# Kernel tuning notes

Hardware: AMD Instinct MI355X
Metric: run time of the kernel (lower is better)

The kernel has to match this reference:

```python
import jax, jax.numpy as jnp
import numpy as np

B, L, D = 4, 2048, 512
H, DK = 8, 64          # n_heads, d_k = d_model // n_heads
DF = 2048              # d_ff
W = 9                  # window_size (odd so padding w//2 keeps L windows)


def setup_inputs() -> dict:
    key = jax.random.key(0)
    ks = jax.random.split(key, 12)
    s = 0.02
    p = lambda k, shp: (jax.random.normal(k, shp, jnp.float32) * s)
    return {
        "x": jax.random.normal(ks[0], (B, L, D), jnp.float32),
        "Wq": p(ks[1], (D, D)), "bq": jnp.zeros((D,), jnp.float32),
        "Wk": p(ks[2], (D, D)), "bk": jnp.zeros((D,), jnp.float32),
        "Wv": p(ks[3], (D, D)), "bv": jnp.zeros((D,), jnp.float32),
        "Wo": p(ks[4], (D, D)), "bo": jnp.zeros((D,), jnp.float32),
        "W1": p(ks[5], (D, DF)), "b1": jnp.zeros((DF,), jnp.float32),
        "W2": p(ks[6], (DF, D)), "b2": jnp.zeros((D,), jnp.float32),
        "g1": jnp.ones((D,), jnp.float32), "be1": jnp.zeros((D,), jnp.float32),
        "g2": jnp.ones((D,), jnp.float32), "be2": jnp.zeros((D,), jnp.float32),
    }


def _layer_norm(x, g, b, eps=1e-5):
    m = jnp.mean(x, axis=-1, keepdims=True)
    v = jnp.var(x, axis=-1, keepdims=True)
    return (x - m) * jax.lax.rsqrt(v + eps) * g + b


def reference(x, Wq, bq, Wk, bk, Wv, bv, Wo, bo, W1, b1, W2, b2, g1, be1, g2, be2):
    b, l, d = x.shape
    pad = W // 2
    padded = jnp.pad(x, ((0, 0), (pad, pad), (0, 0)))          # (B, L+W-1, D)
    idx = jnp.arange(l)[:, None] + jnp.arange(W)[None, :]       # (L, W)
    win = padded[:, idx]                                        # (B, L, W, D)

    # per-window full attention (Informer FullAttention, mask_flag=False)
    q = (win @ Wq + bq).reshape(b, l, W, H, DK)
    k = (win @ Wk + bk).reshape(b, l, W, H, DK)
    v = (win @ Wv + bv).reshape(b, l, W, H, DK)
    scale = 1.0 / jnp.sqrt(jnp.float32(DK))
    scores = jnp.einsum('blqhe,blkhe->blhqk', q, k) * scale     # (B, L, H, W, W)
    attn = jax.nn.softmax(scores, axis=-1)
    o = jnp.einsum('blhqk,blkhd->blqhd', attn, v).reshape(b, l, W, d)
    o = o @ Wo + bo                                             # (B, L, W, D)
    new_x = jnp.mean(o, axis=2)                                 # mean-pool over window

    x1 = _layer_norm(x + new_x, g1, be1)

    # pointwise conv FFN (kernel_size=1 Conv1d == Linear), exact GELU
    h = jax.nn.gelu(x1 @ W1 + b1, approximate=False)
    y = h @ W2 + b2
    return _layer_norm(x1 + y, g2, be2)
```

## Files before the change

kernel.cpp:

```cpp
#include <hip/hip_runtime.h>


typedef unsigned short u16;
typedef __attribute__((ext_vector_type(8))) short short8;
typedef __attribute__((ext_vector_type(4))) float floatx4;

#define DEV static __device__ __forceinline__

DEV float b2f(u16 u) {
  union { unsigned int i; float f; } x; x.i = ((unsigned int)u) << 16; return x.f;
}
DEV u16 f2b(float f) {
  union { float f; unsigned int i; } x; x.f = f;
  unsigned int u = x.i + 0x7fffu + ((x.i >> 16) & 1u);
  return (u16)(u >> 16);
}

#define AS1 __attribute__((address_space(1)))
#define AS3 __attribute__((address_space(3)))
DEV void gload_lds16(const void* g, void* l) {
  __builtin_amdgcn_global_load_lds((const AS1 void*)g, (AS3 void*)l, 16, 0, 0);
}

__global__ __launch_bounds__(256) void prep_weights(
    const float* __restrict__ Wq, const float* __restrict__ Wk,
    const float* __restrict__ Wo, const float* __restrict__ W1,
    const float* __restrict__ W2, const float* __restrict__ Wv,
    u16* __restrict__ WqkvT, u16* __restrict__ WoT,
    u16* __restrict__ W1T, u16* __restrict__ W2T, u16* __restrict__ Wvb) {
  const int bid = blockIdx.x;
  if (bid >= 2816) {
    const int i = (bid - 2816) * 256 + threadIdx.x;
    float4 v = ((const float4*)Wv)[i];
    ushort4 o;
    o.x = f2b(v.x); o.y = f2b(v.y); o.z = f2b(v.z); o.w = f2b(v.w);
    ((ushort4*)Wvb)[i] = o;
    return;
  }
  const float* in; u16* out; int R, C, t;
  if (bid < 256)       { in = Wq; out = WqkvT;          R = 512;  C = 512;  t = bid; }
  else if (bid < 512)  { in = Wk; out = WqkvT + 262144; R = 512;  C = 512;  t = bid - 256; }
  else if (bid < 768)  { in = Wo; out = WoT;            R = 512;  C = 512;  t = bid - 512; }
  else if (bid < 1792) { in = W1; out = W1T;            R = 512;  C = 2048; t = bid - 768; }
  else                 { in = W2; out = W2T;            R = 2048; C = 512;  t = bid - 1792; }
  const int tpr = C >> 5;
  const int bc = (t % tpr) * 32, br = (t / tpr) * 32;
  __shared__ float tile[32][33];
  const int tx = threadIdx.x & 31, ty = threadIdx.x >> 5;
  #pragma unroll
  for (int i = 0; i < 32; i += 8)
    tile[ty + i][tx] = in[(size_t)(br + ty + i) * C + bc + tx];
  __syncthreads();
  #pragma unroll
  for (int i = 0; i < 32; i += 8)
    out[(size_t)(bc + ty + i) * R + br + tx] = f2b(tile[tx][ty + i]);
}

__global__ __launch_bounds__(256) void bias_prep(
    const float* __restrict__ bq, const float* __restrict__ bk,
    const float* __restrict__ bv, const float* __restrict__ Wo,
    float* __restrict__ o) {
  const int i = blockIdx.x * 256 + threadIdx.x;
  if (i < 512) o[i] = bq[i];
  else if (i < 1024) o[i] = bk[i - 512];
  else if (i < 1536) {
    const int c = i - 1024;
    float s = 0.f;
    for (int j = 0; j < 512; ++j) s += bv[j] * Wo[(size_t)j * 512 + c];
    o[i] = s;
  } else if (i < 2048) o[i] = 0.f;
}

__global__ __launch_bounds__(256) void f2b_vec(
    const float* __restrict__ in, u16* __restrict__ out, int n4) {
  int i = blockIdx.x * 256 + threadIdx.x;
  if (i < n4) {
    float4 v = ((const float4*)in)[i];
    ushort4 o;
    o.x = f2b(v.x); o.y = f2b(v.y); o.z = f2b(v.z); o.w = f2b(v.w);
    ((ushort4*)out)[i] = o;
  }
}

template<int EPI>
__global__ __launch_bounds__(256, 4) void gemm_bt(
    const u16* __restrict__ A, const u16* __restrict__ BT,
    const float* __restrict__ bias, u16* __restrict__ C, u16* __restrict__ C2,
    int M, int N, int lda, int kb) {
  __shared__ __align__(16) u16 As[3][4096];
  __shared__ __align__(16) u16 Bs[3][2048];
  const int tid = threadIdx.x;
  const int w = tid >> 6, l = tid & 63;
  const int l15 = l & 15, l4 = l >> 4;
  const int wr = w & 1, wc = w >> 1;

  const int gx = (int)gridDim.x, gy = (int)gridDim.y;
  int id = ((int)blockIdx.z * gy + (int)blockIdx.y) * gx + (int)blockIdx.x;
  const int nwg = gx * gy * (int)gridDim.z;
  if ((nwg & 7) == 0) { const int cpx = nwg >> 3; id = (id & 7) * cpx + (id >> 3); }
  const int bx = id % gx; const int r1 = id / gx;
  const int by = r1 % gy; const int bz = r1 / gy;
  const int bm = by * 128, bn = bx * 64;
  const int koff = bz * kb;

  const int row0 = tid >> 2;
  const int kc0 = ((((tid & 3) - ((tid >> 3) & 3)) & 3)) * 8;
  const u16* gA = A  + (size_t)(bm + row0) * lda + koff + kc0;
  const u16* gB = BT + (size_t)(bn + row0) * lda + koff + kc0;
  const size_t a1 = (size_t)64 * lda;
  const int sd = w * 512 + l * 8;

  const int rg8 = ((l4 + ((l15 >> 1) & 3)) & 3) * 8;
  const int aBase = (wr * 64 + l15) * 32 + rg8;
  const int bBase = (wc * 32 + l15) * 32 + rg8;

  floatx4 acc[4][2] = {};
  const int nt = kb >> 5;

  auto stage = [&](int t, int buf) {
    const u16* a = gA + (size_t)t * 32;
    const u16* b = gB + (size_t)t * 32;
    gload_lds16(a,      &As[buf][sd]);
    gload_lds16(a + a1, &As[buf][2048 + sd]);
    gload_lds16(b,      &Bs[buf][sd]);
  };

  stage(0, 0);
  stage(1, 1);
  asm volatile("s_waitcnt vmcnt(3)" ::: "memory");
  __builtin_amdgcn_s_barrier();
  asm volatile("" ::: "memory");

  int cur = 0;
  for (int t = 0; t < nt; ++t) {
    int sb = cur + 2; if (sb >= 3) sb -= 3;
    const bool pf = (t + 2 < nt);
    if (pf) stage(t + 2, sb);

    short8 af[4], bf[2];
    #pragma unroll
    for (int m = 0; m < 4; ++m) af[m] = *(const short8*)(&As[cur][aBase + m * 512]);
    #pragma unroll
    for (int n = 0; n < 2; ++n) bf[n] = *(const short8*)(&Bs[cur][bBase + n * 512]);
    #pragma unroll
    for (int m = 0; m < 4; ++m)
      #pragma unroll
      for (int n = 0; n < 2; ++n)
        acc[m][n] = __builtin_amdgcn_mfma_f32_16x16x32_bf16(af[m], bf[n], acc[m][n], 0, 0, 0);

    if (pf) asm volatile("s_waitcnt vmcnt(3)" ::: "memory");
    else    asm volatile("s_waitcnt vmcnt(0)" ::: "memory");
    __builtin_amdgcn_s_barrier();
    asm volatile("" ::: "memory");

    cur = (cur == 2) ? 0 : cur + 1;
  }

  const int col0 = bn + wc * 32 + l15;
  if (EPI <= 1) {
    float bvv[2];
    #pragma unroll
    for (int n = 0; n < 2; ++n) bvv[n] = bias[col0 + n * 16];
    #pragma unroll
    for (int m = 0; m < 4; ++m) {
      #pragma unroll
      for (int ri = 0; ri < 4; ++ri) {
        const size_t row = (size_t)(bm + wr * 64 + m * 16 + l4 * 4 + ri);
        u16* cp = C + row * N + col0;
        #pragma unroll
        for (int n = 0; n < 2; ++n) {
          float vv = acc[m][n][ri] + bvv[n];
          if (EPI == 1) vv = 0.5f * vv * (1.0f + erff(vv * 0.70710678118654752f));
          cp[n * 16] = f2b(vv);
        }
      }
    }
  } else {
    u16* o = (bz == 0) ? C : C2;
    #pragma unroll
    for (int m = 0; m < 4; ++m) {
      #pragma unroll
      for (int ri = 0; ri < 4; ++ri) {
        const size_t row = (size_t)(bm + wr * 64 + m * 16 + l4 * 4 + ri);
        u16* cp = o + row * N + col0;
        #pragma unroll
        for (int n = 0; n < 2; ++n) cp[n * 16] = f2b(acc[m][n][ri]);
      }
    }
  }
}

#define ATL 32
#define ART (ATL + 8)

__global__ __launch_bounds__(256) void attn_band(
    const u16* __restrict__ QKV, const float* __restrict__ bqkv,
    const float* __restrict__ bo, u16* __restrict__ newx) {
  __shared__ __align__(16) u16 S3[3][ART][72];
  __shared__ float Gb[ART][18];
  __shared__ float Sm[ART][81];
  __shared__ float Wb[ATL][9];

  const int tid = threadIdx.x;
  const int bid = ((int)blockIdx.x & 7) * 256 + ((int)blockIdx.x >> 3);
  const int h = bid & 7;
  const int chunk = (bid >> 3) & 63;
  const int b = bid >> 9;
  const int l0 = chunk * ATL;

  for (int idx = tid; idx < ART * 24; idx += 256) {
    const int ti = idx / 24, c = idx % 24;
    const int slice = c >> 3, d8 = (c & 7) * 8;
    const int col = slice * 512 + h * 64 + d8;
    const int t = l0 - 4 + ti;
    short8 v;
    if ((unsigned)t < 2048u) {
      v = *(const short8*)(QKV + ((size_t)((b << 11) | t)) * 1536 + col);
    } else {
      #pragma unroll
      for (int j = 0; j < 8; ++j) v[j] = (short)f2b(bqkv[col + j]);
    }
    *(short8*)(&S3[slice][ti][d8]) = v;
  }
  __syncthreads();

  for (int task = tid; task < ART * 17; task += 256) {
    const int ti = task / 17, j = task % 17;
    const int ui = ti + j - 8;
    if ((unsigned)ui < (unsigned)ART) {
      float a = 0.f;
      #pragma unroll
      for (int d0 = 0; d0 < 64; d0 += 8) {
        short8 qv = *(const short8*)(&S3[0][ti][d0]);
        short8 kv = *(const short8*)(&S3[1][ui][d0]);
        #pragma unroll
        for (int jj = 0; jj < 8; ++jj) a += b2f((u16)qv[jj]) * b2f((u16)kv[jj]);
      }
      Gb[ti][j] = a * 0.125f;
    }
  }
  __syncthreads();

  for (int task = tid; task < ART * 9; task += 256) {
    const int ti = task / 9, qw = task % 9;
    const int li = ti - qw;
    if ((unsigned)li < (unsigned)ATL) {
      float m = -1e30f;
      #pragma unroll
      for (int kw = 0; kw < 9; ++kw) m = fmaxf(m, Gb[ti][kw - qw + 8]);
      float e[9], s = 0.f;
      #pragma unroll
      for (int kw = 0; kw < 9; ++kw) { e[kw] = expf(Gb[ti][kw - qw + 8] - m); s += e[kw]; }
      const float inv = 1.f / s;
      #pragma unroll
      for (int kw = 0; kw < 9; ++kw) Sm[ti][qw * 9 + kw] = e[kw] * inv;
    }
  }
  __syncthreads();

  for (int task = tid; task < ATL * 9; task += 256) {
    const int li = task / 9, kw = task % 9;
    float s = 0.f;
    #pragma unroll
    for (int qw = 0; qw < 9; ++qw) s += Sm[li + qw][qw * 9 + kw];
    Wb[li][kw] = s * (1.f / 9.f);
  }
  __syncthreads();

  {
    const int li = tid >> 3, d8 = (tid & 7) * 8;
    float w[9];
    #pragma unroll
    for (int kw = 0; kw < 9; ++kw) w[kw] = Wb[li][kw];
    float a[8] = {};
    #pragma unroll
    for (int kw = 0; kw < 9; ++kw) {
      short8 vv = *(const short8*)(&S3[2][li + kw][d8]);
      #pragma unroll
      for (int jj = 0; jj < 8; ++jj) a[jj] += w[kw] * b2f((u16)vv[jj]);
    }
    short8 o;
    #pragma unroll
    for (int jj = 0; jj < 8; ++jj) o[jj] = (short)f2b(a[jj] + bo[h * 64 + d8 + jj]);
    const int l = l0 + li;
    *(short8*)(newx + ((size_t)((b << 11) | l)) * 512 + h * 64 + d8) = o;
  }
}

template<int MODE>
__global__ __launch_bounds__(256) void ln_kernel(
    const u16* __restrict__ a, const u16* __restrict__ bsrc,
    const u16* __restrict__ csrc, const float* __restrict__ bias,
    const float* __restrict__ g, const float* __restrict__ be,
    u16* __restrict__ outb, float* __restrict__ outf) {
  const int wave = threadIdx.x >> 6, lane = threadIdx.x & 63;
  const size_t row = (size_t)blockIdx.x * 4 + wave;
  const size_t base = row * 512 + lane * 8;
  const int gi = lane * 8;
  float v[8];
  short8 a8 = *(const short8*)(a + base);
  short8 b8 = *(const short8*)(bsrc + base);
  #pragma unroll
  for (int j = 0; j < 8; ++j) v[j] = b2f((u16)a8[j]) + b2f((u16)b8[j]);
  if (MODE == 1) {
    short8 c8 = *(const short8*)(csrc + base);
    #pragma unroll
    for (int j = 0; j < 8; ++j) v[j] += b2f((u16)c8[j]) + bias[gi + j];
  }

  float s = 0.f;
  #pragma unroll
  for (int j = 0; j < 8; ++j) s += v[j];
  #pragma unroll
  for (int off = 32; off >= 1; off >>= 1) s += __shfl_xor(s, off, 64);
  const float mean = s * (1.f / 512.f);
  float sq = 0.f;
  #pragma unroll
  for (int j = 0; j < 8; ++j) { float d = v[j] - mean; sq += d * d; }
  #pragma unroll
  for (int off = 32; off >= 1; off >>= 1) sq += __shfl_xor(sq, off, 64);
  const float rs = rsqrtf(sq * (1.f / 512.f) + 1e-5f);

  if (MODE == 0) {
    short8 o;
    #pragma unroll
    for (int j = 0; j < 8; ++j)
      o[j] = (short)f2b((v[j] - mean) * rs * g[gi + j] + be[gi + j]);
    *(short8*)(outb + base) = o;
  } else {
    float4 o0, o1;
    o0.x = (v[0] - mean) * rs * g[gi + 0] + be[gi + 0];
    o0.y = (v[1] - mean) * rs * g[gi + 1] + be[gi + 1];
    o0.z = (v[2] - mean) * rs * g[gi + 2] + be[gi + 2];
    o0.w = (v[3] - mean) * rs * g[gi + 3] + be[gi + 3];
    o1.x = (v[4] - mean) * rs * g[gi + 4] + be[gi + 4];
    o1.y = (v[5] - mean) * rs * g[gi + 5] + be[gi + 5];
    o1.z = (v[6] - mean) * rs * g[gi + 6] + be[gi + 6];
    o1.w = (v[7] - mean) * rs * g[gi + 7] + be[gi + 7];
    *(float4*)(outf + base) = o0;
    *(float4*)(outf + base + 4) = o1;
  }
}

extern "C" void kernel_launch(void* const* d_in, const int* in_sizes, int n_in,
                              void* d_out, int out_size, void* d_ws, size_t ws_size,
                              hipStream_t stream) {
  const float* x   = (const float*)d_in[0];
  const float* Wq  = (const float*)d_in[1];
  const float* bq  = (const float*)d_in[2];
  const float* Wk  = (const float*)d_in[3];
  const float* bk  = (const float*)d_in[4];
  const float* Wv  = (const float*)d_in[5];
  const float* bv  = (const float*)d_in[6];
  const float* Wo  = (const float*)d_in[7];
  const float* bo  = (const float*)d_in[8];
  const float* W1  = (const float*)d_in[9];
  const float* b1  = (const float*)d_in[10];
  const float* W2  = (const float*)d_in[11];
  const float* b2  = (const float*)d_in[12];
  const float* g1  = (const float*)d_in[13];
  const float* be1 = (const float*)d_in[14];
  const float* g2  = (const float*)d_in[15];
  const float* be2 = (const float*)d_in[16];

  char* w = (char*)d_ws;
  u16*   xb    = (u16*)  (w + 0);
  u16*   WqkvT = (u16*)  (w + 8388608);
  u16*   WoT   = (u16*)  (w + 9961472);
  u16*   W1T   = (u16*)  (w + 10485760);
  u16*   W2T   = (u16*)  (w + 12582912);
  float* bqkv  = (float*)(w + 14680064);
  u16*   Wvb   = (u16*)  (w + 14688256);
  u16*   QKV   = (u16*)  (w + 15212544);
  u16*   hbuf  = QKV;
  u16*   newx  = (u16*)  (w + 48766976);
  u16*   x1b   = (u16*)  (w + 57155584);
  u16*   WvoT  = WqkvT + 524288;
  u16*   yp0   = newx;
  u16*   yp1   = xb;

  prep_weights<<<3072, 256, 0, stream>>>(Wq, Wk, Wo, W1, W2, Wv,
                                         WqkvT, WoT, W1T, W2T, Wvb);
  bias_prep<<<8, 256, 0, stream>>>(bq, bk, bv, Wo, bqkv);
  f2b_vec<<<4096, 256, 0, stream>>>(x, xb, 1048576);
  gemm_bt<0><<<dim3(8, 4, 1), 256, 0, stream>>>(WoT, Wvb, bqkv + 1536, WvoT, nullptr,
                                                512, 512, 512, 512);
  gemm_bt<0><<<dim3(24, 64, 1), 256, 0, stream>>>(xb, WqkvT, bqkv, QKV, nullptr,
                                                  8192, 1536, 512, 512);
  attn_band<<<2048, 256, 0, stream>>>(QKV, bqkv, bo, newx);
  ln_kernel<0><<<2048, 256, 0, stream>>>(xb, newx, nullptr, nullptr, g1, be1, x1b, nullptr);
  gemm_bt<1><<<dim3(32, 64, 1), 256, 0, stream>>>(x1b, W1T, b1, hbuf, nullptr,
                                                  8192, 2048, 512, 512);
  gemm_bt<2><<<dim3(8, 64, 2), 256, 0, stream>>>(hbuf, W2T, nullptr, yp0, yp1,
                                                 8192, 512, 2048, 1024);
  ln_kernel<1><<<2048, 256, 0, stream>>>(x1b, yp0, yp1, b2, g2, be2, nullptr, (float*)d_out);
}
```

Baseline: 164.1 us.

## Replace 128x64 GEMM with 256x256-tile, 512-thread, 4-stage pipelined kernel

Swaps the 128x64-tile bf16 MFMA GEMM for a 256x256-tile kernel run by 8 waves. Each wave computes a 128x64 sub-tile with an 8x4 accumulator array. The K-loop becomes a 4-deep LDS ring, with A and B staging split across two half-steps, setprio around the MFMA bursts and explicit vmcnt waits. The aim is more operand reuse per LDS byte and better overlap of loads with compute. In exchange it uses much more LDS and registers per block and launches far fewer workgroups (for example 192 for QKV and 128 for FFN2), which may leave CUs idle.

Result: slower. 212.8 us (+29.7%).

```diff
diff --git a/kernel.cpp b/kernel.cpp
--- a/kernel.cpp
+++ b/kernel.cpp
@@ -82,17 +82,67 @@
   }
 }
 
+#define STAGE_A(j) do { \
+    const u16* _a = gA + (size_t)(j) * 32; \
+    gload_lds16(_a,         &LA[(j) & 3][sd]); \
+    gload_lds16(_a + rstep, &LA[(j) & 3][4096 + sd]); \
+  } while (0)
+#define STAGE_B(j) do { \
+    const u16* _b = gB + (size_t)(j) * 32; \
+    gload_lds16(_b,         &LB[(j) & 3][sd]); \
+    gload_lds16(_b + rstep, &LB[(j) & 3][4096 + sd]); \
+  } while (0)
+
+#define TILE_BODY(kk, DOSTAGE, WAITASM) do { \
+    const u16* la = &LA[(kk) & 3][0]; \
+    const u16* lb = &LB[(kk) & 3][0]; \
+     \
+    if (DOSTAGE) STAGE_A((kk) + 3); \
+    asm volatile(WAITASM ::: "memory"); \
+    __builtin_amdgcn_s_barrier(); \
+    short8 af[4], bf[4]; \
+    _Pragma("unroll") \
+    for (int m = 0; m < 4; ++m) af[m] = *(const short8*)(la + aOff[m]); \
+    _Pragma("unroll") \
+    for (int n = 0; n < 4; ++n) bf[n] = *(const short8*)(lb + bOff[n]); \
+    asm volatile("s_waitcnt lgkmcnt(0)" ::: "memory"); \
+    __builtin_amdgcn_sched_barrier(0); \
+    __builtin_amdgcn_s_setprio(1); \
+    _Pragma("unroll") \
+    for (int m = 0; m < 4; ++m) \
+      _Pragma("unroll") \
+      for (int n = 0; n < 4; ++n) \
+        acc[m][n] = __builtin_amdgcn_mfma_f32_16x16x32_bf16(af[m], bf[n], acc[m][n], 0, 0, 0); \
+    __builtin_amdgcn_s_setprio(0); \
+    __builtin_amdgcn_s_barrier(); \
+     \
+    if (DOSTAGE) STAGE_B((kk) + 3); \
+    short8 a2[4]; \
+    _Pragma("unroll") \
+    for (int m = 0; m < 4; ++m) a2[m] = *(const short8*)(la + aOff[m + 4]); \
+    asm volatile("s_waitcnt lgkmcnt(0)" ::: "memory"); \
+    __builtin_amdgcn_sched_barrier(0); \
+    __builtin_amdgcn_s_setprio(1); \
+    _Pragma("unroll") \
+    for (int m = 0; m < 4; ++m) \
+      _Pragma("unroll") \
+      for (int n = 0; n < 4; ++n) \
+        acc[m + 4][n] = __builtin_amdgcn_mfma_f32_16x16x32_bf16(a2[m], bf[n], acc[m + 4][n], 0, 0, 0); \
+    __builtin_amdgcn_s_setprio(0); \
+    __builtin_amdgcn_s_barrier(); \
+  } while (0)
+
 template<int EPI>
-__global__ __launch_bounds__(256, 4) void gemm_bt(
+__global__ __launch_bounds__(512, 2) void gemm256(
     const u16* __restrict__ A, const u16* __restrict__ BT,
     const float* __restrict__ bias, u16* __restrict__ C, u16* __restrict__ C2,
     int M, int N, int lda, int kb) {
-  __shared__ __align__(16) u16 As[3][4096];
-  __shared__ __align__(16) u16 Bs[3][2048];
+  __shared__ __align__(16) u16 LA[4][8192];
+  __shared__ __align__(16) u16 LB[4][8192];
   const int tid = threadIdx.x;
   const int w = tid >> 6, l = tid & 63;
   const int l15 = l & 15, l4 = l >> 4;
-  const int wr = w & 1, wc = w >> 1;
+  const int wr = w >> 2, wc = w & 3;
 
   const int gx = (int)gridDim.x, gy = (int)gridDim.y;
   int id = ((int)blockIdx.z * gy + (int)blockIdx.y) * gx + (int)blockIdx.x;
@@ -100,75 +150,49 @@
   if ((nwg & 7) == 0) { const int cpx = nwg >> 3; id = (id & 7) * cpx + (id >> 3); }
   const int bx = id % gx; const int r1 = id / gx;
   const int by = r1 % gy; const int bz = r1 / gy;
-  const int bm = by * 128, bn = bx * 64;
+  const int bm = by * 256, bn = bx * 256;
   const int koff = bz * kb;
 
   const int row0 = tid >> 2;
   const int kc0 = ((((tid & 3) - ((tid >> 3) & 3)) & 3)) * 8;
   const u16* gA = A  + (size_t)(bm + row0) * lda + koff + kc0;
   const u16* gB = BT + (size_t)(bn + row0) * lda + koff + kc0;
-  const size_t a1 = (size_t)64 * lda;
-  const int sd = w * 512 + l * 8;
+  const size_t rstep = (size_t)128 * lda;
+  const int sd = tid * 8;
 
   const int rg8 = ((l4 + ((l15 >> 1) & 3)) & 3) * 8;
-  const int aBase = (wr * 64 + l15) * 32 + rg8;
-  const int bBase = (wc * 32 + l15) * 32 + rg8;
-
-  floatx4 acc[4][2] = {};
+  int aOff[8], bOff[4];
+  #pragma unroll
+  for (int m = 0; m < 8; ++m) aOff[m] = (wr * 128 + m * 16 + l15) * 32 + rg8;
+  #pragma unroll
+  for (int n = 0; n < 4; ++n) bOff[n] = (wc * 64 + n * 16 + l15) * 32 + rg8;
+
+  floatx4 acc[8][4] = {};
   const int nt = kb >> 5;
 
-  auto stage = [&](int t, int buf) {
-    const u16* a = gA + (size_t)t * 32;
-    const u16* b = gB + (size_t)t * 32;
-    gload_lds16(a,      &As[buf][sd]);
-    gload_lds16(a + a1, &As[buf][2048 + sd]);
-    gload_lds16(b,      &Bs[buf][sd]);
-  };
-
-  stage(0, 0);
-  stage(1, 1);
-  asm volatile("s_waitcnt vmcnt(3)" ::: "memory");
-  __builtin_amdgcn_s_barrier();
-  asm volatile("" ::: "memory");
-
-  int cur = 0;
-  for (int t = 0; t < nt; ++t) {
-    int sb = cur + 2; if (sb >= 3) sb -= 3;
-    const bool pf = (t + 2 < nt);
-    if (pf) stage(t + 2, sb);
-
-    short8 af[4], bf[2];
-    #pragma unroll
-    for (int m = 0; m < 4; ++m) af[m] = *(const short8*)(&As[cur][aBase + m * 512]);
-    #pragma unroll
-    for (int n = 0; n < 2; ++n) bf[n] = *(const short8*)(&Bs[cur][bBase + n * 512]);
-    #pragma unroll
-    for (int m = 0; m < 4; ++m)
-      #pragma unroll
-      for (int n = 0; n < 2; ++n)
-        acc[m][n] = __builtin_amdgcn_mfma_f32_16x16x32_bf16(af[m], bf[n], acc[m][n], 0, 0, 0);
-
-    if (pf) asm volatile("s_waitcnt vmcnt(3)" ::: "memory");
-    else    asm volatile("s_waitcnt vmcnt(0)" ::: "memory");
-    __builtin_amdgcn_s_barrier();
-    asm volatile("" ::: "memory");
-
-    cur = (cur == 2) ? 0 : cur + 1;
-  }
-
-  const int col0 = bn + wc * 32 + l15;
+  STAGE_A(0); STAGE_B(0);
+  STAGE_A(1); STAGE_B(1);
+  STAGE_A(2); STAGE_B(2);
+
+  for (int k = 0; k < nt - 3; ++k)
+    TILE_BODY(k, true, "s_waitcnt vmcnt(10)");
+  TILE_BODY(nt - 3, false, "s_waitcnt vmcnt(8)");
+  TILE_BODY(nt - 2, false, "s_waitcnt vmcnt(4)");
+  TILE_BODY(nt - 1, false, "s_waitcnt vmcnt(0)");
+
+  const int col0 = bn + wc * 64 + l15;
   if (EPI <= 1) {
-    float bvv[2];
-    #pragma unroll
-    for (int n = 0; n < 2; ++n) bvv[n] = bias[col0 + n * 16];
-    #pragma unroll
-    for (int m = 0; m < 4; ++m) {
+    float bvv[4];
+    #pragma unroll
+    for (int n = 0; n < 4; ++n) bvv[n] = bias[col0 + n * 16];
+    #pragma unroll
+    for (int m = 0; m < 8; ++m) {
       #pragma unroll
       for (int ri = 0; ri < 4; ++ri) {
-        const size_t row = (size_t)(bm + wr * 64 + m * 16 + l4 * 4 + ri);
+        const size_t row = (size_t)(bm + wr * 128 + m * 16 + l4 * 4 + ri);
         u16* cp = C + row * N + col0;
         #pragma unroll
-        for (int n = 0; n < 2; ++n) {
+        for (int n = 0; n < 4; ++n) {
           float vv = acc[m][n][ri] + bvv[n];
           if (EPI == 1) vv = 0.5f * vv * (1.0f + erff(vv * 0.70710678118654752f));
           cp[n * 16] = f2b(vv);
@@ -178,13 +202,13 @@
   } else {
     u16* o = (bz == 0) ? C : C2;
     #pragma unroll
-    for (int m = 0; m < 4; ++m) {
+    for (int m = 0; m < 8; ++m) {
       #pragma unroll
       for (int ri = 0; ri < 4; ++ri) {
-        const size_t row = (size_t)(bm + wr * 64 + m * 16 + l4 * 4 + ri);
+        const size_t row = (size_t)(bm + wr * 128 + m * 16 + l4 * 4 + ri);
         u16* cp = o + row * N + col0;
         #pragma unroll
-        for (int n = 0; n < 2; ++n) cp[n * 16] = f2b(acc[m][n][ri]);
+        for (int n = 0; n < 4; ++n) cp[n * 16] = f2b(acc[m][n][ri]);
       }
     }
   }
@@ -383,15 +407,15 @@
                                          WqkvT, WoT, W1T, W2T, Wvb);
   bias_prep<<<8, 256, 0, stream>>>(bq, bk, bv, Wo, bqkv);
   f2b_vec<<<4096, 256, 0, stream>>>(x, xb, 1048576);
-  gemm_bt<0><<<dim3(8, 4, 1), 256, 0, stream>>>(WoT, Wvb, bqkv + 1536, WvoT, nullptr,
+  gemm256<0><<<dim3(2, 2, 1), 512, 0, stream>>>(WoT, Wvb, bqkv + 1536, WvoT, nullptr,
                                                 512, 512, 512, 512);
-  gemm_bt<0><<<dim3(24, 64, 1), 256, 0, stream>>>(xb, WqkvT, bqkv, QKV, nullptr,
-                                                  8192, 1536, 512, 512);
+  gemm256<0><<<dim3(6, 32, 1), 512, 0, stream>>>(xb, WqkvT, bqkv, QKV, nullptr,
+                                                 8192, 1536, 512, 512);
   attn_band<<<2048, 256, 0, stream>>>(QKV, bqkv, bo, newx);
   ln_kernel<0><<<2048, 256, 0, stream>>>(xb, newx, nullptr, nullptr, g1, be1, x1b, nullptr);
-  gemm_bt<1><<<dim3(32, 64, 1), 256, 0, stream>>>(x1b, W1T, b1, hbuf, nullptr,
-                                                  8192, 2048, 512, 512);
-  gemm_bt<2><<<dim3(8, 64, 2), 256, 0, stream>>>(hbuf, W2T, nullptr, yp0, yp1,
+  gemm256<1><<<dim3(8, 32, 1), 512, 0, stream>>>(x1b, W1T, b1, hbuf, nullptr,
+                                                 8192, 2048, 512, 512);
+  gemm256<2><<<dim3(2, 32, 2), 512, 0, stream>>>(hbuf, W2T, nullptr, yp0, yp1,
                                                  8192, 512, 2048, 1024);
   ln_kernel<1><<<2048, 256, 0, stream>>>(x1b, yp0, yp1, b2, g2, be2, nullptr, (float*)d_out);
 }
```
